# Performance work log

Measured on AMD Instinct MI355X. Metric: run time of the kernel, lower is better.

The kernel has to match this reference:

```python
import jax, jax.numpy as jnp
import numpy as np

B, S, E, H = 4, 2048, 1024, 16
D = E // H  # key_size


def setup_inputs() -> dict:
    key = jax.random.key(0)
    ks = jax.random.split(key, 6)
    s = 1.0 / np.sqrt(E)
    return {
        "X": jax.random.normal(ks[0], (B, S, E), dtype=jnp.float32),
        "Wq": jax.random.uniform(ks[1], (E, E), jnp.float32, -s, s),
        "Wk": jax.random.uniform(ks[2], (E, E), jnp.float32, -s, s),
        "Wv": jax.random.uniform(ks[3], (E, E), jnp.float32, -s, s),
        "Wo": jax.random.uniform(ks[4], (E, E), jnp.float32, -s, s),
        "bo": jax.random.uniform(ks[5], (E,), jnp.float32, -s, s),
    }


def reference(X, Wq, Wk, Wv, Wo, bo):
    # Linear layers: y = x @ W^T (torch convention), no bias for q/k/v
    def split(x):  # [B,S,E] -> [B,H,S,D]
        return x.reshape(B, S, H, D).transpose(0, 2, 1, 3)

    q = split(X @ Wq.T)
    k = split(X @ Wk.T)
    v = split(X @ Wv.T)
    scale = jnp.asarray(np.sqrt(D), dtype=X.dtype)
    scores = jnp.einsum("bhqd,bhkd->bhqk", q, k) / scale
    probs = jax.nn.softmax(scores, axis=-1)
    ctx = jnp.einsum("bhqk,bhkd->bhqd", probs, v)
    out = ctx.transpose(0, 2, 1, 3).reshape(B, S, E)
    return out @ Wo.T + bo
```

## Files before the change

kernel.cpp:

```cpp
#include <hip/hip_runtime.h>
#include <hip/hip_bf16.h>

typedef short bf16x8 __attribute__((ext_vector_type(8)));
typedef float f32x4  __attribute__((ext_vector_type(4)));

__device__ __forceinline__ short f2bf(float f) {
    union { float f; unsigned u; } x; x.f = f;
    unsigned r = x.u + 0x7fffu + ((x.u >> 16) & 1u);
    return (short)(r >> 16);
}

__device__ __forceinline__ unsigned rbits(float f) {
    union { float f; unsigned u; } x; x.f = f;
    return x.u + 0x8000u;
}
__device__ __forceinline__ int pack2(float a, float b) {
    return (int)__builtin_amdgcn_perm(rbits(b), rbits(a), 0x07060302u);
}

__device__ __forceinline__ f32x4 mfma32k(bf16x8 a, bf16x8 b, f32x4 c) {
    return __builtin_amdgcn_mfma_f32_16x16x32_bf16(a, b, c, 0, 0, 0);
}

#define GLDS16(g, l)                                                            \
    __builtin_amdgcn_global_load_lds(                                           \
        (const __attribute__((address_space(1))) void*)(g),                     \
        (__attribute__((address_space(3))) void*)(l), 16, 0, 0)

static constexpr int Bb = 4, Ss = 2048, Ee = 1024, Hh = 16, Dd = 64;
static constexpr int Mrows = Bb * Ss;
static constexpr float CL2 = 0.1803368801111204f;

__global__ void cvt_all(const float* __restrict__ X,  const float* __restrict__ Wq,
                        const float* __restrict__ Wk, const float* __restrict__ Wv,
                        const float* __restrict__ Wo,
                        short* __restrict__ Xb, short* __restrict__ Wqk,
                        short* __restrict__ Wvb, short* __restrict__ Wob) {
    int bid = blockIdx.x;
    const float* src; short* dst; int off; float scale = 1.0f;
    if (bid < 8192) {
        src = X; dst = Xb; off = bid * 1024;
    } else {
        int wsel = (bid - 8192) >> 10;
        off = ((bid - 8192) & 1023) * 1024;
        if      (wsel == 0) { src = Wq; dst = Wqk;                scale = CL2; }
        else if (wsel == 1) { src = Wk; dst = Wqk + Ee * Ee; }
        else if (wsel == 2) { src = Wv; dst = Wvb; }
        else                { src = Wo; dst = Wob; }
    }
    int i = off + threadIdx.x * 4;
    float4 v = *(const float4*)(src + i);
    short4 o;
    o.x = f2bf(v.x * scale); o.y = f2bf(v.y * scale);
    o.z = f2bf(v.z * scale); o.w = f2bf(v.w * scale);
    *(short4*)(dst + i) = o;
}

template<bool BIAS_F32OUT, bool PERMC>
__global__ __launch_bounds__(256, 2)
void gemm_bt(const short* __restrict__ A, int lda,
             const short* __restrict__ Bm, int ldb,
             void* __restrict__ C, int ldc,
             const float* __restrict__ bias, int K) {
    __shared__ __align__(16) short sA[2 * 128 * 32];
    __shared__ __align__(16) short sB[2 * 128 * 32];
    const int t = threadIdx.x, w = t >> 6, l = t & 63;
    const int lane16 = l & 15, quad = l >> 4;
    const int wm = (w >> 1) * 64, wn = (w & 1) * 64;
    const int bm = blockIdx.x, bn = blockIdx.y;

    f32x4 acc[4][4] = {};
    const short* Ab = A + (size_t)bm * 128 * lda;
    const short* Bbp = Bm + (size_t)bn * 128 * ldb;

    for (int k0 = 0; k0 < K; k0 += 64) {
#pragma unroll
        for (int p = 0; p < 4; ++p) {
            int c = p * 256 + t;
            int panel = c >> 9, row = (c >> 2) & 127, cs = c & 3;
            int col = k0 + panel * 32 + cs * 8;
            short* ldst = (p * 256 + w * 64) * 8 + (short*)nullptr;
            GLDS16(Ab + (size_t)row * lda + col, sA + (p * 256 + w * 64) * 8);
            GLDS16(Bbp + (size_t)row * ldb + col, sB + (p * 256 + w * 64) * 8);
            (void)ldst;
        }
        __syncthreads();
#pragma unroll
        for (int s2 = 0; s2 < 2; ++s2) {
            bf16x8 af[4], bfr[4];
#pragma unroll
            for (int i = 0; i < 4; ++i) {
                af[i]  = *(const bf16x8*)(sA + s2 * 4096 + (wm + i * 16 + lane16) * 32 + quad * 8);
                bfr[i] = *(const bf16x8*)(sB + s2 * 4096 + (wn + i * 16 + lane16) * 32 + quad * 8);
            }
#pragma unroll
            for (int i = 0; i < 4; ++i)
#pragma unroll
                for (int j = 0; j < 4; ++j)
                    acc[i][j] = mfma32k(af[i], bfr[j], acc[i][j]);
        }
        __syncthreads();
    }

    const int sEven = (lane16 >> 2) * 8 + (lane16 & 3);
#pragma unroll
    for (int i = 0; i < 4; ++i)
#pragma unroll
        for (int j = 0; j < 4; ++j) {
            int row = bm * 128 + wm + i * 16 + quad * 4;
            int col = bn * 128 + wn + j * 16 + lane16;
            if (BIAS_F32OUT) {
                float bv = bias[col];
                float* Cf = (float*)C;
#pragma unroll
                for (int r = 0; r < 4; ++r)
                    Cf[(size_t)(row + r) * ldc + col] = acc[i][j][r] + bv;
            } else {
                if (PERMC) col = (col & ~31) | (sEven + (j & 1) * 4);
                short* Cb = (short*)C;
#pragma unroll
                for (int r = 0; r < 4; ++r)
                    Cb[(size_t)(row + r) * ldc + col] = f2bf(acc[i][j][r]);
            }
        }
}

__global__ __launch_bounds__(256, 4)
void attn_kernel(const short* __restrict__ QK, const short* __restrict__ VT,
                 short* __restrict__ CTX) {
    __shared__ __align__(16) short sK[8192];
    __shared__ __align__(16) short sV[8192];
    const int t = threadIdx.x, w = t >> 6, l = t & 63;
    const int lane16 = l & 15, quad = l >> 4;
    const int bh = blockIdx.x, qt = blockIdx.y;
    const int b = bh >> 4, h = bh & 15;

    const short* Qb = QK + ((size_t)(b * 2048 + qt * 128)) * 2048 + h * 64;
    const short* Kb = QK + ((size_t)(b * 2048)) * 2048 + 1024 + h * 64;
    const short* Vb = VT + ((size_t)(h * 64)) * 8192 + (size_t)b * 2048;

#pragma unroll
    for (int p = 0; p < 4; ++p) {
        int c = p * 256 + t;
        int half = c >> 9, row = (c >> 2) & 127, dq = c & 3;
        GLDS16(Qb + (size_t)row * 2048 + half * 32 + dq * 8, sK + (p * 256 + w * 64) * 8);
    }
    __syncthreads();
    bf16x8 qf[2][2];
#pragma unroll
    for (int mt = 0; mt < 2; ++mt)
#pragma unroll
        for (int ks = 0; ks < 2; ++ks)
            qf[mt][ks] = *(const bf16x8*)(sK + ks * 4096 + (w * 32 + mt * 16 + lane16) * 32 + quad * 8);
    __syncthreads();

    f32x4 l4[2] = {};
    f32x4 o[2][4] = {};

    for (int kt = 0; kt < 16; ++kt) {
        const short* KbT = Kb + (size_t)kt * 128 * 2048;
        const short* VbT = Vb + kt * 128;
#pragma unroll
        for (int p = 0; p < 4; ++p) {
            int c = p * 256 + t;
            int half = c >> 9, row = (c >> 2) & 127, dq = c & 3;
            GLDS16(KbT + (size_t)row * 2048 + half * 32 + dq * 8, sK + (p * 256 + w * 64) * 8);
        }
#pragma unroll
        for (int p = 0; p < 4; ++p) {
            int c = p * 256 + t;
            int kb = c >> 8, d = (c >> 2) & 63, kq = c & 3;
            GLDS16(VbT + (size_t)d * 8192 + kb * 32 + kq * 8, sV + (p * 256 + w * 64) * 8);
        }
        __syncthreads();

#pragma unroll
        for (int a = 0; a < 4; ++a) {
            f32x4 sc[2][2] = {};
#pragma unroll
            for (int sub = 0; sub < 2; ++sub) {
                int nt = a * 2 + sub;
                bf16x8 kf0 = *(const bf16x8*)(sK + (nt * 16 + lane16) * 32 + quad * 8);
                bf16x8 kf1 = *(const bf16x8*)(sK + 4096 + (nt * 16 + lane16) * 32 + quad * 8);
#pragma unroll
                for (int mt = 0; mt < 2; ++mt) {
                    sc[mt][sub] = mfma32k(kf0, qf[mt][0], sc[mt][sub]);
                    sc[mt][sub] = mfma32k(kf1, qf[mt][1], sc[mt][sub]);
                }
            }
            bf16x8 pf[2];
#pragma unroll
            for (int mt = 0; mt < 2; ++mt) {
                union { int i[4]; bf16x8 v; } u;
#pragma unroll
                for (int sub = 0; sub < 2; ++sub) {
                    f32x4 e;
#pragma unroll
                    for (int r = 0; r < 4; ++r)
                        e[r] = __builtin_amdgcn_exp2f(sc[mt][sub][r]);
                    l4[mt] += e;
                    u.i[sub * 2]     = pack2(e[0], e[1]);
                    u.i[sub * 2 + 1] = pack2(e[2], e[3]);
                }
                pf[mt] = u.v;
            }
#pragma unroll
            for (int dt = 0; dt < 4; ++dt) {
                bf16x8 vf = *(const bf16x8*)(sV + a * 2048 + (dt * 16 + lane16) * 32 + quad * 8);
#pragma unroll
                for (int mt = 0; mt < 2; ++mt)
                    o[mt][dt] = mfma32k(pf[mt], vf, o[mt][dt]);
            }
        }
        __syncthreads();
    }

    float l_i[2];
#pragma unroll
    for (int mt = 0; mt < 2; ++mt) {
        l_i[mt] = (l4[mt][0] + l4[mt][1]) + (l4[mt][2] + l4[mt][3]);
        l_i[mt] += __shfl_xor(l_i[mt], 16);
        l_i[mt] += __shfl_xor(l_i[mt], 32);
    }
#pragma unroll
    for (int mt = 0; mt < 2; ++mt)
#pragma unroll
        for (int r = 0; r < 4; ++r) {
            float lr = __shfl(l_i[mt], quad * 4 + r);
            float inv = 1.0f / lr;
            int row = b * 2048 + qt * 128 + w * 32 + mt * 16 + quad * 4 + r;
#pragma unroll
            for (int dt = 0; dt < 4; ++dt)
                CTX[(size_t)row * 1024 + h * 64 + dt * 16 + lane16] = f2bf(o[mt][dt][r] * inv);
        }
}

extern "C" void kernel_launch(void* const* d_in, const int* in_sizes, int n_in,
                              void* d_out, int out_size, void* d_ws, size_t ws_size,
                              hipStream_t stream) {
    const float* X  = (const float*)d_in[0];
    const float* Wq = (const float*)d_in[1];
    const float* Wk = (const float*)d_in[2];
    const float* Wv = (const float*)d_in[3];
    const float* Wo = (const float*)d_in[4];
    const float* bo = (const float*)d_in[5];
    float* out = (float*)d_out;

    char* ws = (char*)d_ws;
    constexpr size_t OFF_XB  = 0;
    constexpr size_t OFF_WQK = OFF_XB  + (size_t)Mrows * Ee * 2;
    constexpr size_t OFF_WV  = OFF_WQK + (size_t)2 * Ee * Ee * 2;
    constexpr size_t OFF_WO  = OFF_WV  + (size_t)Ee * Ee * 2;
    constexpr size_t OFF_QK  = OFF_WO  + (size_t)Ee * Ee * 2;
    constexpr size_t OFF_VT  = OFF_QK  + (size_t)Mrows * 2048 * 2;
    constexpr size_t OFF_CTX = OFF_VT  + (size_t)Ee * Mrows * 2;
    short* Xb   = (short*)(ws + OFF_XB);
    short* Wqk  = (short*)(ws + OFF_WQK);
    short* Wvb  = (short*)(ws + OFF_WV);
    short* Wob  = (short*)(ws + OFF_WO);
    short* QKb  = (short*)(ws + OFF_QK);
    short* VTb  = (short*)(ws + OFF_VT);
    short* CTX  = (short*)(ws + OFF_CTX);

    cvt_all<<<12288, 256, 0, stream>>>(X, Wq, Wk, Wv, Wo, Xb, Wqk, Wvb, Wob);

    gemm_bt<false, false><<<dim3(Mrows / 128, 2048 / 128), 256, 0, stream>>>(
        Xb, Ee, Wqk, Ee, QKb, 2048, nullptr, Ee);

    gemm_bt<false, true><<<dim3(Ee / 128, Mrows / 128), 256, 0, stream>>>(
        Wvb, Ee, Xb, Ee, VTb, Mrows, nullptr, Ee);

    attn_kernel<<<dim3(Bb * Hh, Ss / 128), 256, 0, stream>>>(QKb, VTb, CTX);

    gemm_bt<true, false><<<dim3(Mrows / 128, Ee / 128), 256, 0, stream>>>(
        CTX, Ee, Wob, Ee, out, Ee, bo, Ee);
}
```

Baseline: 275.1 us.

## Merge QK and V projection GEMMs into one launch, shrink K-step, MFMA row sums

The QK and V^T projection GEMMs now run as a single launch that picks its operands by block index, which removes one kernel launch and lets both jobs share one grid. Both GEMMs now use a K-step of 32 with half-size LDS tiles. That raises possible occupancy but doubles the number of barriers per K loop. In attention, softmax row sums are computed with an MFMA against a ones vector instead of vector adds plus cross-lane shuffles. Global load offsets are also precomputed and the pointers advanced incrementally.

New measurement: 259.0 us. -5.9%, faster.

```diff
diff --git a/kernel.cpp b/kernel.cpp
--- a/kernel.cpp
+++ b/kernel.cpp
@@ -56,72 +56,121 @@
     *(short4*)(dst + i) = o;
 }
 
-template<bool BIAS_F32OUT, bool PERMC>
 __global__ __launch_bounds__(256, 2)
-void gemm_bt(const short* __restrict__ A, int lda,
-             const short* __restrict__ Bm, int ldb,
-             void* __restrict__ C, int ldc,
-             const float* __restrict__ bias, int K) {
-    __shared__ __align__(16) short sA[2 * 128 * 32];
-    __shared__ __align__(16) short sB[2 * 128 * 32];
+void gemm_fused(const short* __restrict__ A0, const short* __restrict__ B0,
+                short* __restrict__ C0,
+                const short* __restrict__ A1, const short* __restrict__ B1,
+                short* __restrict__ C1, int split) {
+    __shared__ __align__(16) short sA[128 * 32];
+    __shared__ __align__(16) short sB[128 * 32];
+    const int t = threadIdx.x, w = t >> 6, l = t & 63;
+    const int lane16 = l & 15, quad = l >> 4;
+    const int wm = (w >> 1) * 64, wn = (w & 1) * 64;
+
+    int bid = blockIdx.x;
+    const short *A, *Bm; short* C;
+    int bm, bn, ldc; bool perm;
+    if (bid < split) {
+        bm = bid & 63; bn = bid >> 6;
+        A = A0; Bm = B0; C = C0; ldc = 2048; perm = false;
+    } else {
+        int id = bid - split;
+        bm = id & 7; bn = id >> 3;
+        A = A1; Bm = B1; C = C1; ldc = 8192; perm = true;
+    }
+
+    f32x4 acc[4][4] = {};
+    const short* Ab  = A  + (size_t)bm * 128 * 1024;
+    const short* Bbp = Bm + (size_t)bn * 128 * 1024;
+    const int s0 = w * 64 + l;
+    const int ldsOff = (w * 64) * 8;
+
+    for (int k0 = 0; k0 < 1024; k0 += 32) {
+#pragma unroll
+        for (int p = 0; p < 2; ++p) {
+            int s = p * 256 + s0;
+            int row = s >> 2, cs = s & 3;
+            GLDS16(Ab + (size_t)row * 1024 + k0 + cs * 8, sA + p * 2048 + ldsOff);
+            GLDS16(Bbp + (size_t)row * 1024 + k0 + cs * 8, sB + p * 2048 + ldsOff);
+        }
+        __syncthreads();
+        bf16x8 af[4], bfr[4];
+#pragma unroll
+        for (int i = 0; i < 4; ++i) {
+            af[i]  = *(const bf16x8*)(sA + (wm + i * 16 + lane16) * 32 + quad * 8);
+            bfr[i] = *(const bf16x8*)(sB + (wn + i * 16 + lane16) * 32 + quad * 8);
+        }
+#pragma unroll
+        for (int i = 0; i < 4; ++i)
+#pragma unroll
+            for (int j = 0; j < 4; ++j)
+                acc[i][j] = mfma32k(af[i], bfr[j], acc[i][j]);
+        __syncthreads();
+    }
+
+    const int sEven = (lane16 >> 2) * 8 + (lane16 & 3);
+#pragma unroll
+    for (int i = 0; i < 4; ++i)
+#pragma unroll
+        for (int j = 0; j < 4; ++j) {
+            int row = bm * 128 + wm + i * 16 + quad * 4;
+            int col = bn * 128 + wn + j * 16 + lane16;
+            if (perm) col = (col & ~31) | (sEven + (j & 1) * 4);
+#pragma unroll
+            for (int r = 0; r < 4; ++r)
+                C[(size_t)(row + r) * ldc + col] = f2bf(acc[i][j][r]);
+        }
+}
+
+__global__ __launch_bounds__(256, 2)
+void gemm_out(const short* __restrict__ A, const short* __restrict__ Bm,
+              float* __restrict__ C, const float* __restrict__ bias) {
+    __shared__ __align__(16) short sA[128 * 32];
+    __shared__ __align__(16) short sB[128 * 32];
     const int t = threadIdx.x, w = t >> 6, l = t & 63;
     const int lane16 = l & 15, quad = l >> 4;
     const int wm = (w >> 1) * 64, wn = (w & 1) * 64;
     const int bm = blockIdx.x, bn = blockIdx.y;
 
     f32x4 acc[4][4] = {};
-    const short* Ab = A + (size_t)bm * 128 * lda;
-    const short* Bbp = Bm + (size_t)bn * 128 * ldb;
-
-    for (int k0 = 0; k0 < K; k0 += 64) {
-#pragma unroll
-        for (int p = 0; p < 4; ++p) {
-            int c = p * 256 + t;
-            int panel = c >> 9, row = (c >> 2) & 127, cs = c & 3;
-            int col = k0 + panel * 32 + cs * 8;
-            short* ldst = (p * 256 + w * 64) * 8 + (short*)nullptr;
-            GLDS16(Ab + (size_t)row * lda + col, sA + (p * 256 + w * 64) * 8);
-            GLDS16(Bbp + (size_t)row * ldb + col, sB + (p * 256 + w * 64) * 8);
-            (void)ldst;
-        }
-        __syncthreads();
-#pragma unroll
-        for (int s2 = 0; s2 < 2; ++s2) {
-            bf16x8 af[4], bfr[4];
-#pragma unroll
-            for (int i = 0; i < 4; ++i) {
-                af[i]  = *(const bf16x8*)(sA + s2 * 4096 + (wm + i * 16 + lane16) * 32 + quad * 8);
-                bfr[i] = *(const bf16x8*)(sB + s2 * 4096 + (wn + i * 16 + lane16) * 32 + quad * 8);
-            }
-#pragma unroll
-            for (int i = 0; i < 4; ++i)
-#pragma unroll
-                for (int j = 0; j < 4; ++j)
-                    acc[i][j] = mfma32k(af[i], bfr[j], acc[i][j]);
-        }
-        __syncthreads();
-    }
-
-    const int sEven = (lane16 >> 2) * 8 + (lane16 & 3);
+    const short* Ab  = A  + (size_t)bm * 128 * 1024;
+    const short* Bbp = Bm + (size_t)bn * 128 * 1024;
+    const int s0 = w * 64 + l;
+    const int ldsOff = (w * 64) * 8;
+
+    for (int k0 = 0; k0 < 1024; k0 += 32) {
+#pragma unroll
+        for (int p = 0; p < 2; ++p) {
+            int s = p * 256 + s0;
+            int row = s >> 2, cs = s & 3;
+            GLDS16(Ab + (size_t)row * 1024 + k0 + cs * 8, sA + p * 2048 + ldsOff);
+            GLDS16(Bbp + (size_t)row * 1024 + k0 + cs * 8, sB + p * 2048 + ldsOff);
+        }
+        __syncthreads();
+        bf16x8 af[4], bfr[4];
+#pragma unroll
+        for (int i = 0; i < 4; ++i) {
+            af[i]  = *(const bf16x8*)(sA + (wm + i * 16 + lane16) * 32 + quad * 8);
+            bfr[i] = *(const bf16x8*)(sB + (wn + i * 16 + lane16) * 32 + quad * 8);
+        }
+#pragma unroll
+        for (int i = 0; i < 4; ++i)
+#pragma unroll
+            for (int j = 0; j < 4; ++j)
+                acc[i][j] = mfma32k(af[i], bfr[j], acc[i][j]);
+        __syncthreads();
+    }
+
 #pragma unroll
     for (int i = 0; i < 4; ++i)
 #pragma unroll
         for (int j = 0; j < 4; ++j) {
             int row = bm * 128 + wm + i * 16 + quad * 4;
             int col = bn * 128 + wn + j * 16 + lane16;
-            if (BIAS_F32OUT) {
-                float bv = bias[col];
-                float* Cf = (float*)C;
-#pragma unroll
-                for (int r = 0; r < 4; ++r)
-                    Cf[(size_t)(row + r) * ldc + col] = acc[i][j][r] + bv;
-            } else {
-                if (PERMC) col = (col & ~31) | (sEven + (j & 1) * 4);
-                short* Cb = (short*)C;
-#pragma unroll
-                for (int r = 0; r < 4; ++r)
-                    Cb[(size_t)(row + r) * ldc + col] = f2bf(acc[i][j][r]);
-            }
+            float bv = bias[col];
+#pragma unroll
+            for (int r = 0; r < 4; ++r)
+                C[(size_t)(row + r) * 1024 + col] = acc[i][j][r] + bv;
         }
 }
 
@@ -136,15 +185,20 @@
     const int b = bh >> 4, h = bh & 15;
 
     const short* Qb = QK + ((size_t)(b * 2048 + qt * 128)) * 2048 + h * 64;
-    const short* Kb = QK + ((size_t)(b * 2048)) * 2048 + 1024 + h * 64;
     const short* Vb = VT + ((size_t)(h * 64)) * 8192 + (size_t)b * 2048;
-
+    const int ldsOff = (w * 64) * 8;
+
+    int off_kq[4], off_v[4];
 #pragma unroll
     for (int p = 0; p < 4; ++p) {
         int c = p * 256 + t;
-        int half = c >> 9, row = (c >> 2) & 127, dq = c & 3;
-        GLDS16(Qb + (size_t)row * 2048 + half * 32 + dq * 8, sK + (p * 256 + w * 64) * 8);
-    }
+        off_kq[p] = ((c >> 2) & 127) * 2048 + (c >> 9) * 32 + (c & 3) * 8;
+        off_v[p]  = ((c >> 2) & 63) * 8192 + (c >> 8) * 32 + (c & 3) * 8;
+    }
+
+#pragma unroll
+    for (int p = 0; p < 4; ++p)
+        GLDS16(Qb + off_kq[p], sK + p * 2048 + ldsOff);
     __syncthreads();
     bf16x8 qf[2][2];
 #pragma unroll
@@ -154,24 +208,23 @@
             qf[mt][ks] = *(const bf16x8*)(sK + ks * 4096 + (w * 32 + mt * 16 + lane16) * 32 + quad * 8);
     __syncthreads();
 
-    f32x4 l4[2] = {};
+    const short one = (short)0x3F80;
+    const bf16x8 ONE8 = {one, one, one, one, one, one, one, one};
+    f32x4 lacc[2] = {};
     f32x4 o[2][4] = {};
 
+    const short* kptr = QK + ((size_t)(b * 2048)) * 2048 + 1024 + h * 64;
+    const short* vptr = Vb;
+
     for (int kt = 0; kt < 16; ++kt) {
-        const short* KbT = Kb + (size_t)kt * 128 * 2048;
-        const short* VbT = Vb + kt * 128;
-#pragma unroll
-        for (int p = 0; p < 4; ++p) {
-            int c = p * 256 + t;
-            int half = c >> 9, row = (c >> 2) & 127, dq = c & 3;
-            GLDS16(KbT + (size_t)row * 2048 + half * 32 + dq * 8, sK + (p * 256 + w * 64) * 8);
-        }
-#pragma unroll
-        for (int p = 0; p < 4; ++p) {
-            int c = p * 256 + t;
-            int kb = c >> 8, d = (c >> 2) & 63, kq = c & 3;
-            GLDS16(VbT + (size_t)d * 8192 + kb * 32 + kq * 8, sV + (p * 256 + w * 64) * 8);
-        }
+#pragma unroll
+        for (int p = 0; p < 4; ++p)
+            GLDS16(kptr + off_kq[p], sK + p * 2048 + ldsOff);
+#pragma unroll
+        for (int p = 0; p < 4; ++p)
+            GLDS16(vptr + off_v[p], sV + p * 2048 + ldsOff);
+        kptr += (size_t)128 * 2048;
+        vptr += 128;
         __syncthreads();
 
 #pragma unroll
@@ -198,13 +251,15 @@
 #pragma unroll
                     for (int r = 0; r < 4; ++r)
                         e[r] = __builtin_amdgcn_exp2f(sc[mt][sub][r]);
-                    l4[mt] += e;
                     u.i[sub * 2]     = pack2(e[0], e[1]);
                     u.i[sub * 2 + 1] = pack2(e[2], e[3]);
                 }
                 pf[mt] = u.v;
             }
 #pragma unroll
+            for (int mt = 0; mt < 2; ++mt)
+                lacc[mt] = mfma32k(pf[mt], ONE8, lacc[mt]);
+#pragma unroll
             for (int dt = 0; dt < 4; ++dt) {
                 bf16x8 vf = *(const bf16x8*)(sV + a * 2048 + (dt * 16 + lane16) * 32 + quad * 8);
 #pragma unroll
@@ -215,19 +270,11 @@
         __syncthreads();
     }
 
-    float l_i[2];
-#pragma unroll
-    for (int mt = 0; mt < 2; ++mt) {
-        l_i[mt] = (l4[mt][0] + l4[mt][1]) + (l4[mt][2] + l4[mt][3]);
-        l_i[mt] += __shfl_xor(l_i[mt], 16);
-        l_i[mt] += __shfl_xor(l_i[mt], 32);
-    }
 #pragma unroll
     for (int mt = 0; mt < 2; ++mt)
 #pragma unroll
         for (int r = 0; r < 4; ++r) {
-            float lr = __shfl(l_i[mt], quad * 4 + r);
-            float inv = 1.0f / lr;
+            float inv = 1.0f / lacc[mt][r];
             int row = b * 2048 + qt * 128 + w * 32 + mt * 16 + quad * 4 + r;
 #pragma unroll
             for (int dt = 0; dt < 4; ++dt)
@@ -264,14 +311,9 @@
 
     cvt_all<<<12288, 256, 0, stream>>>(X, Wq, Wk, Wv, Wo, Xb, Wqk, Wvb, Wob);
 
-    gemm_bt<false, false><<<dim3(Mrows / 128, 2048 / 128), 256, 0, stream>>>(
-        Xb, Ee, Wqk, Ee, QKb, 2048, nullptr, Ee);
-
-    gemm_bt<false, true><<<dim3(Ee / 128, Mrows / 128), 256, 0, stream>>>(
-        Wvb, Ee, Xb, Ee, VTb, Mrows, nullptr, Ee);
+    gemm_fused<<<1536, 256, 0, stream>>>(Xb, Wqk, QKb, Wvb, Xb, VTb, 1024);
 
     attn_kernel<<<dim3(Bb * Hh, Ss / 128), 256, 0, stream>>>(QKb, VTb, CTX);
 
-    gemm_bt<true, false><<<dim3(Mrows / 128, Ee / 128), 256, 0, stream>>>(
-        CTX, Ee, Wob, Ee, out, Ee, bo, Ee);
-}
+    gemm_out<<<dim3(Mrows / 128, Ee / 128), 256, 0, stream>>>(CTX, Wob, out, bo);
+}
```
